# Kernel tuning notes

Measured on AMD Instinct MI355X. Metric: run time of the kernel, lower is better.

## Reference

```python
import jax, jax.numpy as jnp
import numpy as np

# Representation: lvals=[0,1] -> nreps NL=2, dim DIM=1+3=4; mult=8; kqv conv out_mult=3*mult
N, K, EDGE_DIM, HID = 10000, 16, 32, 64
MULT, NL, DIM = 8, 2, 4
OUT_MULT = 3 * MULT
E = N * K
NHEADS = 4
HEAD_DIM = MULT * DIM // NHEADS  # 8


def setup_inputs() -> dict:
    key = jax.random.key(0)
    ks = jax.random.split(key, 9)
    out_flat = NL * NL * MULT * OUT_MULT  # 768
    return {
        "basis1": jax.random.normal(ks[0], (E, DIM, NL), jnp.float32),
        "basis2": jax.random.normal(ks[1], (E, NL, DIM), jnp.float32),
        "edge_feats": jax.random.normal(ks[2], (E, EDGE_DIM), jnp.float32),
        "f": jax.random.normal(ks[3], (N, MULT, DIM), jnp.float32),
        "W1": jax.random.normal(ks[4], (HID, EDGE_DIM), jnp.float32) / np.sqrt(EDGE_DIM).astype(np.float32),
        "b1": jnp.zeros((HID,), jnp.float32),
        "W2": jax.random.normal(ks[5], (out_flat, HID), jnp.float32) / np.sqrt(HID).astype(np.float32),
        "b2": jnp.zeros((out_flat,), jnp.float32),
        "neighbor_idx": jax.random.randint(ks[6], (N, K), 0, N, dtype=jnp.int32),
    }


def reference(basis1, basis2, edge_feats, f, W1, b1, W2, b2, neighbor_idx):
    src = neighbor_idx.reshape(-1)  # (E,) source node per edge
    # RadialWeight: 2-layer MLP edge_feats -> per-edge TP weights (E, NL*OUT_MULT, NL*MULT)
    h = jax.nn.relu(edge_feats @ W1.T + b1)
    rw = (h @ W2.T + b2).reshape(E, NL * OUT_MULT, NL * MULT)
    # EquivariantConvolution: gather + small batched matmuls
    f_src = f[src]  # (E, MULT, DIM)
    tmp = jnp.einsum('emd,edl->eml', f_src, basis1).reshape(E, NL * MULT, 1)
    tmp = (rw @ tmp).reshape(E, OUT_MULT, NL)
    kqv = jnp.einsum('eml,eld->emd', tmp, basis2)  # (E, 3*MULT, DIM)
    # split fused k/q/v along multiplicity (repr_h.rep2.mult = 3*mult)
    k_, q_, v_ = jnp.split(kqv.reshape(N, K, OUT_MULT, DIM), 3, axis=2)  # each (N,K,MULT,DIM)
    k_ = k_.reshape(N, K, NHEADS, HEAD_DIM)
    v_ = v_.reshape(N, K, NHEADS, HEAD_DIM)
    q_node = q_.reshape(N, K, NHEADS, HEAD_DIM).mean(axis=1)  # per-node query (N,H,hd)
    scale = HEAD_DIM ** -0.5
    scores = jnp.einsum('nhd,nkhd->nhk', q_node, k_) * scale  # (N,H,K)
    w = jax.nn.softmax(scores, axis=-1)
    out = jnp.einsum('nhk,nkhd->nhd', w, v_)  # (N,H,hd)
    return out.reshape(N, MULT, DIM)
```

## Files before the change

kernel.cpp:

```cpp
#include <hip/hip_runtime.h>
#include <hip/hip_bf16.h>
#include <math.h>

#define N_NODES 10000
#define KNBR    16
#define EDGEF   32
#define HID     64
#define E_TOT   (N_NODES*KNBR)

#define EPB 128
#define TPB 256
#define NODES_PB 8
#define NSLICE 33
#define CHUNK 4
#define NCHUNK 8

typedef float    f32x4 __attribute__((ext_vector_type(4)));
typedef _Float16 f16x8 __attribute__((ext_vector_type(8)));

#define BF1_HALVES (4*64*8)
#define BF2_HALVES (3*NSLICE*64*8)
#define WS_HALVES  (BF1_HALVES + BF2_HALVES)

__global__ __launch_bounds__(256)
void esa_prep(const float* __restrict__ W1, const float* __restrict__ W2,
              const float* __restrict__ b2, _Float16* __restrict__ wsh)
{
    int i = blockIdx.x * 256 + threadIdx.x;
    if (i >= WS_HALVES) return;
    float v;
    if (i < BF1_HALVES) {
        int j = i & 7, lane = (i >> 3) & 63, t = i >> 9;
        int k = ((lane >> 4) << 3) + j;
        int n = (t << 4) + (lane & 15);
        v = W1[n * EDGEF + k];
    } else {
        int i2 = i - BF1_HALVES;
        int j = i2 & 7, lane = (i2 >> 3) & 63;
        int st = i2 >> 9;
        int s = st % NSLICE, t = st / NSLICE;
        int k = (s << 5) + ((lane >> 4) << 3) + j;
        int n = (t << 4) + (lane & 15);
        if (k < 1024)      v = W2[(n * 16 + (k >> 6)) * HID + (k & 63)];
        else if (k < 1040) v = b2[n * 16 + (k - 1024)];
        else               v = 0.f;
    }
    wsh[i] = (_Float16)v;
}

__device__ __forceinline__ void issue16(const _Float16* g, unsigned char* l) {
    __builtin_amdgcn_global_load_lds(
        (const __attribute__((address_space(1))) void*)g,
        (__attribute__((address_space(3))) void*)(void*)l, 16, 0, 0);
}

__global__ __launch_bounds__(TPB, 3)
void esa_main(const float* __restrict__ basis1, const float* __restrict__ basis2,
              const float* __restrict__ edge_feats, const float* __restrict__ f,
              const float* __restrict__ b1, const int* __restrict__ nbr,
              const _Float16* __restrict__ wsh, float* __restrict__ out)
{
    __shared__ __align__(16) unsigned char smem[53248];
    _Float16* hls = (_Float16*)(smem + 24576);
    _Float16* tpl = (_Float16*)(smem + 43008);
    float*    b2l = (float*)(smem + 47104);
    float*    t2  = (float*)smem;

    const int tid  = threadIdx.x;
    const int eb   = blockIdx.x * EPB;
    const int lane = tid & 63;
    const int w    = tid >> 6;
    const int lo   = lane & 15, hi = lane >> 4;

    const _Float16* Bf2 = wsh + BF1_HALVES;

    #pragma unroll
    for (int j = 0; j < 3; ++j) {
        issue16(Bf2 + ((size_t)((j*NSLICE + (0*CHUNK + w))*64) + lane)*8,
                smem + 0*12288 + (w*3 + j)*1024);
        issue16(Bf2 + ((size_t)((j*NSLICE + (1*CHUNK + w))*64) + lane)*8,
                smem + 1*12288 + (w*3 + j)*1024);
    }

    {
        int el = tid >> 1, hf = tid & 1;
        int e  = eb + el;
        int src = nbr[e];
        const float4* b1p = (const float4*)(basis1 + (size_t)e * 8);
        float4 u0 = b1p[0], u1 = b1p[1];
        float bl0[4] = {u0.x, u0.z, u1.x, u1.z};
        float bl1[4] = {u0.y, u0.w, u1.y, u1.w};
        const float4* fp = (const float4*)(f + (size_t)src * 32 + hf * 16);
        _Float16 tpv[8];
        #pragma unroll
        for (int mm = 0; mm < 4; ++mm) {
            float4 fv = fp[mm];
            float a0 = fv.x*bl0[0] + fv.y*bl0[1] + fv.z*bl0[2] + fv.w*bl0[3];
            float a1 = fv.x*bl1[0] + fv.y*bl1[1] + fv.z*bl1[2] + fv.w*bl1[3];
            tpv[mm*2+0] = (_Float16)a0;
            tpv[mm*2+1] = (_Float16)a1;
        }
        *(f16x8*)(tpl + el*16 + hf*8) = *(f16x8*)tpv;
        float4 b2v = ((const float4*)(basis2 + (size_t)e * 8))[hf];
        *((float4*)(b2l + el*12) + hf) = b2v;
    }

    {
        float b1v[4];
        #pragma unroll
        for (int t = 0; t < 4; ++t) b1v[t] = b1[t*16 + lo];
        f16x8 afr[2];
        #pragma unroll
        for (int mt = 0; mt < 2; ++mt) {
            size_t eg = (size_t)(eb + w*32 + mt*16 + lo);
            const float4* p = (const float4*)(edge_feats + eg*32 + hi*8);
            float4 x0 = p[0], x1 = p[1];
            f16x8 a;
            a[0]=(_Float16)x0.x; a[1]=(_Float16)x0.y; a[2]=(_Float16)x0.z; a[3]=(_Float16)x0.w;
            a[4]=(_Float16)x1.x; a[5]=(_Float16)x1.y; a[6]=(_Float16)x1.z; a[7]=(_Float16)x1.w;
            afr[mt] = a;
        }
        #pragma unroll
        for (int t = 0; t < 4; ++t) {
            f16x8 bfr = *(const f16x8*)(wsh + ((size_t)(t*64 + lane)) * 8);
            #pragma unroll
            for (int mt = 0; mt < 2; ++mt) {
                f32x4 acc = {0.f, 0.f, 0.f, 0.f};
                acc = __builtin_amdgcn_mfma_f32_16x16x32_f16(afr[mt], bfr, acc, 0, 0, 0);
                #pragma unroll
                for (int r = 0; r < 4; ++r) {
                    float hv = acc[r] + b1v[t];
                    hv = hv > 0.f ? hv : 0.f;
                    int el = w*32 + mt*16 + hi*4 + r;
                    hls[el*72 + t*16 + lo] = (_Float16)hv;
                }
            }
        }
    }
    __syncthreads();

    f32x4 acc[2][3];
    #pragma unroll
    for (int mt = 0; mt < 2; ++mt)
        #pragma unroll
        for (int t = 0; t < 3; ++t)
            acc[mt][t] = (f32x4){0.f, 0.f, 0.f, 0.f};

    const int e0 = w*32 + lo, e1 = e0 + 16;
    f16x8 tp0a = *(const f16x8*)(tpl + e0*16);
    f16x8 tp0b = *(const f16x8*)(tpl + e0*16 + 8);
    f16x8 tp1a = *(const f16x8*)(tpl + e1*16);
    f16x8 tp1b = *(const f16x8*)(tpl + e1*16 + 8);
    f16x8 h0f[2], h1f[2];
    h0f[0] = *(const f16x8*)(hls + e0*72 + hi*8);
    h0f[1] = *(const f16x8*)(hls + e0*72 + 32 + hi*8);
    h1f[0] = *(const f16x8*)(hls + e1*72 + hi*8);
    h1f[1] = *(const f16x8*)(hls + e1*72 + 32 + hi*8);

    #pragma unroll
    for (int c = 0; c < NCHUNK; ++c) {
        const _Float16* buf = (const _Float16*)(smem + (c & 1)*12288);
        #pragma unroll
        for (int sc = 0; sc < CHUNK; ++sc) {
            const int s  = c*CHUNK + sc;
            const int cc = s >> 1;
            const int sh = s & 1;
            f16x8 bfr[3];
            #pragma unroll
            for (int t = 0; t < 3; ++t)
                bfr[t] = *(const f16x8*)(buf + ((sc*3 + t)*64 + lane)*8);
            _Float16 s0 = (cc < 8) ? tp0a[cc & 7] : tp0b[cc & 7];
            _Float16 s1 = (cc < 8) ? tp1a[cc & 7] : tp1b[cc & 7];
            f16x8 a0 = h0f[sh] * (f16x8){s0,s0,s0,s0,s0,s0,s0,s0};
            f16x8 a1 = h1f[sh] * (f16x8){s1,s1,s1,s1,s1,s1,s1,s1};
            #pragma unroll
            for (int t = 0; t < 3; ++t) {
                acc[0][t] = __builtin_amdgcn_mfma_f32_16x16x32_f16(a0, bfr[t], acc[0][t], 0, 0, 0);
                acc[1][t] = __builtin_amdgcn_mfma_f32_16x16x32_f16(a1, bfr[t], acc[1][t], 0, 0, 0);
            }
        }
        __syncthreads();
        if (c + 2 < NCHUNK) {
            const int s = (c + 2)*CHUNK + w;
            #pragma unroll
            for (int j = 0; j < 3; ++j)
                issue16(Bf2 + ((size_t)((j*NSLICE + s)*64) + lane)*8,
                        smem + (c & 1)*12288 + (w*3 + j)*1024);
        }
    }

    {
        f16x8 z = {(_Float16)0,(_Float16)0,(_Float16)0,(_Float16)0,
                   (_Float16)0,(_Float16)0,(_Float16)0,(_Float16)0};
        f16x8 a0 = (hi == 0) ? tp0a : (hi == 1) ? tp0b : z;
        f16x8 a1 = (hi == 0) ? tp1a : (hi == 1) ? tp1b : z;
        #pragma unroll
        for (int t = 0; t < 3; ++t) {
            f16x8 bfr = *(const f16x8*)(Bf2 + ((size_t)((t*NSLICE + 32)*64 + lane)) * 8);
            acc[0][t] = __builtin_amdgcn_mfma_f32_16x16x32_f16(a0, bfr, acc[0][t], 0, 0, 0);
            acc[1][t] = __builtin_amdgcn_mfma_f32_16x16x32_f16(a1, bfr, acc[1][t], 0, 0, 0);
        }
    }

    #pragma unroll
    for (int mt = 0; mt < 2; ++mt)
        #pragma unroll
        for (int t = 0; t < 3; ++t)
            #pragma unroll
            for (int r = 0; r < 4; ++r)
                t2[(w*32 + mt*16 + hi*4 + r)*52 + t*16 + lo] = acc[mt][t][r];
    __syncthreads();

    const int kk = lane >> 2, hh = lane & 3;
    #pragma unroll
    for (int it = 0; it < 2; ++it) {
        int nl = it*4 + w;
        int node = blockIdx.x * NODES_PB + nl;
        int el = nl*16 + kk;
        const float* trow = t2 + el*52;
        float4 tk = *(const float4*)(trow + hh*4);
        float4 tq = *(const float4*)(trow + 16 + hh*4);
        float4 tv = *(const float4*)(trow + 32 + hh*4);
        float4 bl0 = *(const float4*)(b2l + el*12);
        float4 bl1 = *(const float4*)(b2l + el*12 + 4);
        float k8[8], q8[8], v8[8];
        const float* B0 = (const float*)&bl0;
        const float* B1 = (const float*)&bl1;
        #pragma unroll
        for (int d = 0; d < 4; ++d) {
            k8[d]   = tk.x*B0[d] + tk.y*B1[d];
            k8[4+d] = tk.z*B0[d] + tk.w*B1[d];
            q8[d]   = tq.x*B0[d] + tq.y*B1[d];
            q8[4+d] = tq.z*B0[d] + tq.w*B1[d];
            v8[d]   = tv.x*B0[d] + tv.y*B1[d];
            v8[4+d] = tv.z*B0[d] + tv.w*B1[d];
        }
        float qn[8];
        #pragma unroll
        for (int i = 0; i < 8; ++i) qn[i] = q8[i];
        #pragma unroll
        for (int m = 4; m <= 32; m <<= 1)
            #pragma unroll
            for (int i = 0; i < 8; ++i) qn[i] += __shfl_xor(qn[i], m);
        float s = 0.f;
        #pragma unroll
        for (int i = 0; i < 8; ++i) s += qn[i]*k8[i];
        s *= 0.0220970869120796f;

        float mx = s;
        #pragma unroll
        for (int m = 4; m <= 32; m <<= 1) mx = fmaxf(mx, __shfl_xor(mx, m));
        float ex = __expf(s - mx);
        float den = ex;
        #pragma unroll
        for (int m = 4; m <= 32; m <<= 1) den += __shfl_xor(den, m);
        float wgt = ex / den;

        float o[8];
        #pragma unroll
        for (int i = 0; i < 8; ++i) o[i] = wgt * v8[i];
        #pragma unroll
        for (int m = 4; m <= 32; m <<= 1)
            #pragma unroll
            for (int i = 0; i < 8; ++i) o[i] += __shfl_xor(o[i], m);
        if (kk == 0) {
            float4* dst = (float4*)(out + (size_t)node*32 + hh*8);
            dst[0] = make_float4(o[0], o[1], o[2], o[3]);
            dst[1] = make_float4(o[4], o[5], o[6], o[7]);
        }
    }
}

extern "C" void kernel_launch(void* const* d_in, const int* in_sizes, int n_in,
                              void* d_out, int out_size, void* d_ws, size_t ws_size,
                              hipStream_t stream) {
    const float* basis1     = (const float*)d_in[0];
    const float* basis2     = (const float*)d_in[1];
    const float* edge_feats = (const float*)d_in[2];
    const float* f          = (const float*)d_in[3];
    const float* W1         = (const float*)d_in[4];
    const float* b1         = (const float*)d_in[5];
    const float* W2         = (const float*)d_in[6];
    const float* b2         = (const float*)d_in[7];
    const int*   nbr        = (const int*)d_in[8];
    float* out = (float*)d_out;
    _Float16* wsh = (_Float16*)d_ws;

    esa_prep<<<(WS_HALVES + 255)/256, 256, 0, stream>>>(W1, W2, b2, wsh);
    esa_main<<<E_TOT/EPB, TPB, 0, stream>>>(basis1, basis2, edge_feats, f,
                                            b1, nbr, wsh, out);
}
```

Measured before the change: 111.6 us.

## Keep hidden activations in registers via transposed MFMA, drop LDS staging

```diff
diff --git a/kernel.cpp b/kernel.cpp
--- a/kernel.cpp
+++ b/kernel.cpp
@@ -32,8 +32,9 @@
     if (i < BF1_HALVES) {
         int j = i & 7, lane = (i >> 3) & 63, t = i >> 9;
         int k = ((lane >> 4) << 3) + j;
-        int n = (t << 4) + (lane & 15);
-        v = W1[n * EDGEF + k];
+        int m = lane & 15;
+        int hid = (t & 1)*4 + (m & 3) + 8*(m >> 2) + 32*(t >> 1);
+        v = W1[hid * EDGEF + k];
     } else {
         int i2 = i - BF1_HALVES;
         int j = i2 & 7, lane = (i2 >> 3) & 63;
@@ -54,16 +55,15 @@
         (__attribute__((address_space(3))) void*)(void*)l, 16, 0, 0);
 }
 
-__global__ __launch_bounds__(TPB, 3)
+__global__ __launch_bounds__(TPB, 4)
 void esa_main(const float* __restrict__ basis1, const float* __restrict__ basis2,
               const float* __restrict__ edge_feats, const float* __restrict__ f,
               const float* __restrict__ b1, const int* __restrict__ nbr,
               const _Float16* __restrict__ wsh, float* __restrict__ out)
 {
-    __shared__ __align__(16) unsigned char smem[53248];
-    _Float16* hls = (_Float16*)(smem + 24576);
-    _Float16* tpl = (_Float16*)(smem + 43008);
-    float*    b2l = (float*)(smem + 47104);
+    __shared__ __align__(16) unsigned char smem[34816];
+    _Float16* tpl = (_Float16*)(smem + 24576);
+    float*    b2l = (float*)(smem + 28672);
     float*    t2  = (float*)smem;
 
     const int tid  = threadIdx.x;
@@ -105,10 +105,8 @@
         *((float4*)(b2l + el*12) + hf) = b2v;
     }
 
+    f16x8 hA[2], hB[2];
     {
-        float b1v[4];
-        #pragma unroll
-        for (int t = 0; t < 4; ++t) b1v[t] = b1[t*16 + lo];
         f16x8 afr[2];
         #pragma unroll
         for (int mt = 0; mt < 2; ++mt) {
@@ -122,17 +120,22 @@
         }
         #pragma unroll
         for (int t = 0; t < 4; ++t) {
-            f16x8 bfr = *(const f16x8*)(wsh + ((size_t)(t*64 + lane)) * 8);
+            f16x8 wfr = *(const f16x8*)(wsh + ((size_t)(t*64 + lane)) * 8);
+            float4 bq = *(const float4*)(b1 + (t & 1)*4 + 8*hi + 32*(t >> 1));
+            const float* bqp = (const float*)&bq;
             #pragma unroll
             for (int mt = 0; mt < 2; ++mt) {
                 f32x4 acc = {0.f, 0.f, 0.f, 0.f};
-                acc = __builtin_amdgcn_mfma_f32_16x16x32_f16(afr[mt], bfr, acc, 0, 0, 0);
+                acc = __builtin_amdgcn_mfma_f32_16x16x32_f16(wfr, afr[mt], acc, 0, 0, 0);
                 #pragma unroll
                 for (int r = 0; r < 4; ++r) {
-                    float hv = acc[r] + b1v[t];
+                    float hv = acc[r] + bqp[r];
                     hv = hv > 0.f ? hv : 0.f;
-                    int el = w*32 + mt*16 + hi*4 + r;
-                    hls[el*72 + t*16 + lo] = (_Float16)hv;
+                    _Float16 hx = (_Float16)hv;
+                    if (t == 0)      hA[mt][r]     = hx;
+                    else if (t == 1) hA[mt][4 + r] = hx;
+                    else if (t == 2) hB[mt][r]     = hx;
+                    else             hB[mt][4 + r] = hx;
                 }
             }
         }
@@ -151,11 +154,6 @@
     f16x8 tp0b = *(const f16x8*)(tpl + e0*16 + 8);
     f16x8 tp1a = *(const f16x8*)(tpl + e1*16);
     f16x8 tp1b = *(const f16x8*)(tpl + e1*16 + 8);
-    f16x8 h0f[2], h1f[2];
-    h0f[0] = *(const f16x8*)(hls + e0*72 + hi*8);
-    h0f[1] = *(const f16x8*)(hls + e0*72 + 32 + hi*8);
-    h1f[0] = *(const f16x8*)(hls + e1*72 + hi*8);
-    h1f[1] = *(const f16x8*)(hls + e1*72 + 32 + hi*8);
 
     #pragma unroll
     for (int c = 0; c < NCHUNK; ++c) {
@@ -171,8 +169,8 @@
                 bfr[t] = *(const f16x8*)(buf + ((sc*3 + t)*64 + lane)*8);
             _Float16 s0 = (cc < 8) ? tp0a[cc & 7] : tp0b[cc & 7];
             _Float16 s1 = (cc < 8) ? tp1a[cc & 7] : tp1b[cc & 7];
-            f16x8 a0 = h0f[sh] * (f16x8){s0,s0,s0,s0,s0,s0,s0,s0};
-            f16x8 a1 = h1f[sh] * (f16x8){s1,s1,s1,s1,s1,s1,s1,s1};
+            f16x8 a0 = (sh ? hB[0] : hA[0]) * (f16x8){s0,s0,s0,s0,s0,s0,s0,s0};
+            f16x8 a1 = (sh ? hB[1] : hA[1]) * (f16x8){s1,s1,s1,s1,s1,s1,s1,s1};
             #pragma unroll
             for (int t = 0; t < 3; ++t) {
                 acc[0][t] = __builtin_amdgcn_mfma_f32_16x16x32_f16(a0, bfr[t], acc[0][t], 0, 0, 0);
```

Measured after the change: 110.5 us. Within noise of the previous version (-1.1%).
